# Kernel tuning notes

Measured on AMD Instinct MI355X. Metric: run time of the kernel, lower is better.

The kernel has to match this reference:

```python
import jax, jax.numpy as jnp
import numpy as np
import math

N_HEADS = 16
D_HEAD = 64
D_MODEL = 1024
ROPE_THETA = 10000.0


def setup_inputs() -> dict:
    key = jax.random.key(0)
    k1, k2, k3 = jax.random.split(key, 3)
    B, T = 2, 2048
    x = jax.random.normal(k1, (B, T, D_MODEL), dtype=jnp.float32)
    # torch Linear(in, out) weight has shape (out, in); store transposed (in, out)
    # so forward is x @ w. Scale like default init to keep activations sane.
    w_qkv = jax.random.normal(k2, (D_MODEL, 3 * D_MODEL), dtype=jnp.float32) / math.sqrt(D_MODEL)
    w_o = jax.random.normal(k3, (D_MODEL, D_MODEL), dtype=jnp.float32) / math.sqrt(D_MODEL)
    return {"x": x, "w_qkv": w_qkv, "w_o": w_o}


def _build_rope(T, dtype):
    inv_freq = 1.0 / (ROPE_THETA ** (jnp.arange(0, D_HEAD, 2, dtype=jnp.float32) / D_HEAD))
    t = jnp.arange(T, dtype=jnp.float32)
    freqs = jnp.outer(t, inv_freq)            # [T, D_HEAD/2]
    emb = jnp.concatenate([freqs, freqs], -1)  # [T, D_HEAD]
    return jnp.cos(emb).astype(dtype), jnp.sin(emb).astype(dtype)


def _apply_rope(x, cos, sin):
    # x: [B, T, H, D_HEAD]; cos/sin broadcast as [1, T, 1, D_HEAD]
    x1, x2 = jnp.split(x, 2, axis=-1)
    rotated = jnp.concatenate([-x2, x1], axis=-1)
    return x * cos + rotated * sin


def reference(x, w_qkv, w_o):
    B, T, D = x.shape
    qkv = (x @ w_qkv).reshape(B, T, 3, N_HEADS, D_HEAD)
    q, k, v = qkv[:, :, 0], qkv[:, :, 1], qkv[:, :, 2]  # [B, T, H, Dh]
    cos, sin = _build_rope(T, x.dtype)
    cos = cos[None, :, None, :]
    sin = sin[None, :, None, :]
    q = _apply_rope(q, cos, sin)
    k = _apply_rope(k, cos, sin)
    scale = 1.0 / math.sqrt(D_HEAD)
    # full [B, H, T, T] scores (faithful to the manual matmul-softmax-matmul)
    attn = jnp.einsum("bthd,bshd->bhts", q, k) * scale
    attn = jax.nn.softmax(attn, axis=-1)
    out = jnp.einsum("bhts,bshd->bthd", attn, v).reshape(B, T, D)
    return out @ w_o
```

## Files before the change

### kernel.cpp

```cpp
#include <hip/hip_runtime.h>
#include <cstdint>

typedef unsigned short ushort_t;
typedef __attribute__((ext_vector_type(8))) short v8s;
typedef __attribute__((ext_vector_type(4))) short v4s;
typedef __attribute__((ext_vector_type(2))) unsigned v2u;
typedef __attribute__((ext_vector_type(4))) float v4f;

#define MFMA(a, b, c) __builtin_amdgcn_mfma_f32_16x16x32_bf16(a, b, c, 0, 0, 0)
#define QSCALE 0.18033688011112042f

#define GLL(gp, lp) __builtin_amdgcn_global_load_lds(                        \
    (const __attribute__((address_space(1))) void*)(gp),                     \
    (__attribute__((address_space(3))) void*)(lp), 16, 0, 0)

__device__ __forceinline__ float bf2f(ushort_t u) {
    union { unsigned u; float f; } x; x.u = ((unsigned)u) << 16; return x.f;
}
__device__ __forceinline__ short f2bf(float f) {
    union { float f; unsigned u; } x; x.f = f;
    unsigned r = x.u + 0x7fffu + ((x.u >> 16) & 1u);
    return (short)(r >> 16);
}

__global__ __launch_bounds__(256) void prep(const void* __restrict__ xin,
                                            const void* __restrict__ w1,
                                            const void* __restrict__ w2,
                                            ushort_t* __restrict__ xb,
                                            ushort_t* __restrict__ out1,
                                            ushort_t* __restrict__ out2,
                                            int* __restrict__ flag,
                                            float* __restrict__ tab) {
    __shared__ ushort_t tile[64][65];
    __shared__ int cnt;
    int bid = blockIdx.x, tid = threadIdx.x;

    int isbf = 0;
    if (bid < 3072 || bid == 3328) {
        if (tid == 0) cnt = 0;
        __syncthreads();
        unsigned w = ((const unsigned*)xin)[tid];
        int e = (w >> 7) & 0xFF;
        int hit = ((e >= 96 && e <= 135) || (w & 0xFFFFu) == 0) ? 1 : 0;
        atomicAdd(&cnt, hit);
        __syncthreads();
        isbf = (cnt >= 160) ? 1 : 0;
        if (bid == 3328) {
            if (tid == 0) *flag = isbf;
            return;
        }
    }

    if (bid < 2048) {
        int i = bid * 256 + tid;
        if (isbf) {
            ((v8s*)xb)[i] = ((const v8s*)xin)[i];
        } else {
            const float* xf = (const float*)xin + (size_t)i * 8;
            v8s o;
            #pragma unroll
            for (int j = 0; j < 8; ++j) o[j] = f2bf(xf[j]);
            ((v8s*)xb)[i] = o;
        }
    } else if (bid < 3072) {
        int t = bid - 2048;
        int bxl = t & 63, by = (t >> 6) * 64;
        const void* in; ushort_t* out; int C, bx;
        if (bxl < 48) { in = w1; out = out1; C = 3072; bx = bxl * 64; }
        else          { in = w2; out = out2; C = 1024; bx = (bxl - 48) * 64; }
        const int R = 1024;
        int tx = tid & 63, ty = tid >> 6;
        for (int i = ty; i < 64; i += 4) {
            size_t idx = (size_t)(by + i) * C + bx + tx;
            tile[i][tx] = isbf ? ((const ushort_t*)in)[idx]
                               : (ushort_t)f2bf(((const float*)in)[idx]);
        }
        __syncthreads();
        for (int i = ty; i < 64; i += 4) out[(size_t)(bx + i) * R + by + tx] = tile[tx][i];
    } else {
        int idx = (bid - 3072) * 256 + tid;
        int t = idx >> 5, d = idx & 31;
        float inv_freq = __expf(-(float)d * 0.28782313662425575f);
        float ang = (float)t * inv_freq;
        float sn, cs;
        sincosf(ang, &sn, &cs);
        tab[t * 64 + d]      = bf2f((ushort_t)f2bf(cs));
        tab[t * 64 + 32 + d] = bf2f((ushort_t)f2bf(sn));
    }
}

template <int MODE, int BN>
__global__ __launch_bounds__(256) void gemm_bt(const ushort_t* __restrict__ A,
                                               const ushort_t* __restrict__ BT,
                                               void* __restrict__ C,
                                               const int* __restrict__ flagp,
                                               int M, int N, int K,
                                               ushort_t* __restrict__ Qp,
                                               ushort_t* __restrict__ Kp,
                                               ushort_t* __restrict__ Vp,
                                               const float* __restrict__ tab) {
    constexpr int NJ = BN / 32;
    __shared__ __align__(16) ushort_t As[2][128 * 32];
    __shared__ __align__(16) ushort_t Bs[2][BN * 32];
    int tid = threadIdx.x;
    int lane = tid & 63;
    int lr = lane & 15, lc = lane >> 4;
    int w = tid >> 6;
    int wr = (w >> 1) * 64, wc = (w & 1) * (BN / 2);

    int nx = gridDim.x;
    int orig = blockIdx.y * nx + blockIdx.x;
    int cpx = (nx * gridDim.y) >> 3;
    int swz = (orig & 7) * cpx + (orig >> 3);
    int m0 = (swz / nx) * 128, n0 = (swz % nx) * BN;

    int c0 = tid, c1 = tid + 256;
    int r0 = c0 >> 2, s0 = c0 & 3;
    int r1 = c1 >> 2, s1 = c1 & 3;

    const ushort_t* Ag0 = A + (size_t)(m0 + r0) * K + s0 * 8;
    const ushort_t* Ag1 = A + (size_t)(m0 + r1) * K + s1 * 8;
    const ushort_t* Bg0 = BT + (size_t)(n0 + r0) * K + s0 * 8;
    const ushort_t* Bg1 = BT + (size_t)(n0 + r1) * K + s1 * 8;
    const int aoff0 = w * 512;
    const int aoff1 = 2048 + w * 512;
    const int boff0 = w * 512;
    const int boff1 = 2048 + w * 512;

    v4f acc[4][NJ] = {};

    GLL(Ag0, &As[0][aoff0]);
    GLL(Ag1, &As[0][aoff1]);
    GLL(Bg0, &Bs[0][boff0]);
    if constexpr (BN == 128) GLL(Bg1, &Bs[0][boff1]);
    __syncthreads();

    int buf = 0;
    for (int kt = 0; kt < K; kt += 32) {
        if (kt + 32 < K) {
            int nb = buf ^ 1;
            GLL(Ag0 + kt + 32, &As[nb][aoff0]);
            GLL(Ag1 + kt + 32, &As[nb][aoff1]);
            GLL(Bg0 + kt + 32, &Bs[nb][boff0]);
            if constexpr (BN == 128) GLL(Bg1 + kt + 32, &Bs[nb][boff1]);
        }

        v8s af[4], bfr[NJ];
        #pragma unroll
        for (int i = 0; i < 4; ++i)
            af[i] = *(const v8s*)(&As[buf][0] + (wr + i * 16 + lr) * 32 + lc * 8);
        #pragma unroll
        for (int j = 0; j < NJ; ++j)
            bfr[j] = *(const v8s*)(&Bs[buf][0] + (wc + j * 16 + lr) * 32 + lc * 8);
        #pragma unroll
        for (int i = 0; i < 4; ++i)
            #pragma unroll
            for (int j = 0; j < NJ; ++j)
                acc[i][j] = MFMA(af[i], bfr[j], acc[i][j]);

        __syncthreads();
        buf ^= 1;
    }

    if (MODE == 1) {
        int store_f32 = (*flagp == 0);
        #pragma unroll
        for (int i = 0; i < 4; ++i)
            #pragma unroll
            for (int j = 0; j < NJ; ++j)
                #pragma unroll
                for (int r = 0; r < 4; ++r) {
                    int row = m0 + wr + i * 16 + lc * 4 + r;
                    int col = n0 + wc + j * 16 + lr;
                    if (store_f32)
                        ((float*)C)[(size_t)row * N + col] = acc[i][j][r];
                    else
                        ((ushort_t*)C)[(size_t)row * N + col] = (ushort_t)f2bf(acc[i][j][r]);
                }
    } else {
        int region = n0 >> 10;
        int h = ((n0 & 1023) + wc) >> 6;
        if (region < 2) {
            const float sc = (region == 0) ? QSCALE : 1.0f;
            ushort_t* dst = (region == 0) ? Qp : Kp;
            #pragma unroll
            for (int i = 0; i < 4; ++i)
                #pragma unroll
                for (int j = 0; j < 2; ++j) {
                    int d = j * 16 + lr;
                    #pragma unroll
                    for (int r = 0; r < 4; ++r) {
                        int tg = m0 + wr + i * 16 + lc * 4 + r;
                        int b = tg >> 11, tt = tg & 2047;
                        float cs = tab[tt * 64 + d], sn = tab[tt * 64 + 32 + d];
                        float x1 = acc[i][j][r], x2 = acc[i][(j + 2) % NJ][r];
                        size_t base = ((size_t)(b * 16 + h) * 2048 + tt) * 64 + d;
                        dst[base]      = (ushort_t)f2bf((x1 * cs - x2 * sn) * sc);
                        dst[base + 32] = (ushort_t)f2bf((x2 * cs + x1 * sn) * sc);
                    }
                }
        } else {
            #pragma unroll
            for (int i = 0; i < 4; ++i)
                #pragma unroll
                for (int j = 0; j < NJ; ++j) {
                    int d = j * 16 + lr;
                    int tg0 = m0 + wr + i * 16 + lc * 4;
                    int b = tg0 >> 11, tt = tg0 & 2047;
                    v4s pk;
                    #pragma unroll
                    for (int r = 0; r < 4; ++r) pk[r] = f2bf(acc[i][j][r]);
                    size_t base = (size_t)(b * 16 + h) * 131072 + (size_t)(tt >> 5) * 2048
                                + (size_t)d * 32 + (tt & 31);
                    *(v4s*)(Vp + base) = pk;
                }
        }
    }
}

__global__ __launch_bounds__(256) void attn(const ushort_t* __restrict__ Qr,
                                            const ushort_t* __restrict__ Kr,
                                            const ushort_t* __restrict__ Vt,
                                            ushort_t* __restrict__ AO) {
    __shared__ __align__(16) char lds[53248];
    int tid = threadIdx.x, lane = tid & 63, W = tid >> 6;
    int lr = lane & 15, lc = lane >> 4;
    int qsub = W & 1, sh = W >> 1;
    int L = blockIdx.x;
    int bh = (L & 7) * 4 + ((L >> 3) & 3);
    int qt = L >> 5;
    int q0 = qt * 128 + qsub * 64;
    int b = bh >> 4, h = bh & 15;
    const ushort_t* Qb = Qr + ((size_t)bh * 2048 + q0) * 64;
    const ushort_t* Kb = Kr + (size_t)bh * 131072 + (size_t)sh * 65536;
    const ushort_t* Vb = Vt + (size_t)bh * 131072 + (size_t)sh * 65536;
    ushort_t* Pw  = (ushort_t*)(lds + 32768 + W * 5120);
    ushort_t* KsG = (ushort_t*)(lds + sh * 16384);
    ushort_t* VsG = (ushort_t*)(lds + sh * 16384 + 8192);

    int gt = tid & 127;
    int c0 = gt, c1 = gt + 128;
    int kr0 = c0 >> 3, kc0 = c0 & 7, kr1 = c1 >> 3, kc1 = c1 & 7;
    const ushort_t* Kg0 = Kb + (size_t)kr0 * 64 + kc0 * 8;
    const ushort_t* Kg1 = Kb + (size_t)kr1 * 64 + kc1 * 8;
    int kl0 = kr0 * 64 + (kc0 ^ (kr0 & 7)) * 8;
    int kl1 = kr1 * 64 + (kc1 ^ (kr1 & 7)) * 8;
    const ushort_t* Vg0 = Vb + (size_t)c0 * 8;
    const ushort_t* Vg1 = Vb + (size_t)c1 * 8;
    int vl0 = c0 * 8, vl1 = c1 * 8;

    v8s qf[4][2];
    #pragma unroll
    for (int jq = 0; jq < 4; ++jq)
        #pragma unroll
        for (int kk = 0; kk < 2; ++kk)
            qf[jq][kk] = *(const v8s*)(Qb + (size_t)(jq * 16 + lr) * 64 + kk * 32 + lc * 8);

    v4f o[4][4] = {};
    float li[4] = {0.f, 0.f, 0.f, 0.f};

    v8s ka = *(const v8s*)(Kg0), kb2 = *(const v8s*)(Kg1);
    v8s va = *(const v8s*)(Vg0), vb2 = *(const v8s*)(Vg1);
    *(v8s*)(KsG + kl0) = ka;
    *(v8s*)(KsG + kl1) = kb2;
    *(v8s*)(VsG + vl0) = va;
    *(v8s*)(VsG + vl1) = vb2;
    ka  = *(const v8s*)(Kg0 + 2048);
    kb2 = *(const v8s*)(Kg1 + 2048);
    va  = *(const v8s*)(Vg0 + 2048);
    vb2 = *(const v8s*)(Vg1 + 2048);
    __syncthreads();

    #pragma unroll 1
    for (int t = 0; t < 32; ++t) {
        int p = t & 1;
        const ushort_t* Kl = KsG + p * 2048;
        const ushort_t* Vl = VsG + p * 2048;

        v8s kf[2][2], vf[4];
        #pragma unroll
        for (int hh = 0; hh < 2; ++hh)
            #pragma unroll
            for (int kk = 0; kk < 2; ++kk)
                kf[hh][kk] = *(const v8s*)(Kl + (hh * 16 + lr) * 64 + (((kk * 4 + lc) ^ (lr & 7)) * 8));
        #pragma unroll
        for (int i = 0; i < 4; ++i)
            vf[i] = *(const v8s*)(Vl + (i * 16 + lr) * 32 + lc * 8);

        v4f St[2][4] = {};
        __builtin_amdgcn_s_setprio(1);
        #pragma unroll
        for (int hh = 0; hh < 2; ++hh)
            #pragma unroll
            for (int jq = 0; jq < 4; ++jq) {
                St[hh][jq] = MFMA(kf[hh][0], qf[jq][0], St[hh][jq]);
                St[hh][jq] = MFMA(kf[hh][1], qf[jq][1], St[hh][jq]);
            }
        __builtin_amdgcn_s_setprio(0);

        if (t + 1 < 32) {
            ushort_t* Kn = KsG + (p ^ 1) * 2048;
            ushort_t* Vn = VsG + (p ^ 1) * 2048;
            *(v8s*)(Kn + kl0) = ka;
            *(v8s*)(Kn + kl1) = kb2;
            *(v8s*)(Vn + vl0) = va;
            *(v8s*)(Vn + vl1) = vb2;
        }
        if (t + 2 < 32) {
            ka  = *(const v8s*)(Kg0 + (size_t)(t + 2) * 2048);
            kb2 = *(const v8s*)(Kg1 + (size_t)(t + 2) * 2048);
            va  = *(const v8s*)(Vg0 + (size_t)(t + 2) * 2048);
            vb2 = *(const v8s*)(Vg1 + (size_t)(t + 2) * 2048);
        }

        #pragma unroll
        for (int jq = 0; jq < 4; ++jq)
            #pragma unroll
            for (int hh = 0; hh < 2; ++hh) {
                #pragma unroll
                for (int r = 0; r < 4; ++r) {
                    float ev = __builtin_amdgcn_exp2f(St[hh][jq][r]);
                    St[hh][jq][r] = ev;
                    li[jq] += ev;
                }
                unsigned d0 = __builtin_amdgcn_perm(__float_as_uint(St[hh][jq][1]),
                                                    __float_as_uint(St[hh][jq][0]), 0x07060302u);
                unsigned d1 = __builtin_amdgcn_perm(__float_as_uint(St[hh][jq][3]),
                                                    __float_as_uint(St[hh][jq][2]), 0x07060302u);
                v2u pk = {d0, d1};
                *(v2u*)(Pw + (jq * 16 + lr) * 40 + hh * 16 + lc * 4) = pk;
            }
        __builtin_amdgcn_s_waitcnt(0xc07f);
        __builtin_amdgcn_s_setprio(1);
        #pragma unroll
        for (int jq = 0; jq < 4; ++jq) {
            v8s pf = *(const v8s*)(Pw + (jq * 16 + lr) * 40 + lc * 8);
            #pragma unroll
            for (int i = 0; i < 4; ++i)
                o[i][jq] = MFMA(vf[i], pf, o[i][jq]);
        }
        __builtin_amdgcn_s_setprio(0);
        __syncthreads();
    }

    #pragma unroll
    for (int jq = 0; jq < 4; ++jq) {
        li[jq] += __shfl_xor(li[jq], 16);
        li[jq] += __shfl_xor(li[jq], 32);
    }
    float* MO = (float*)(lds + qsub * 17408);
    float* Ml = (float*)(lds + 34816 + qsub * 256);
    __syncthreads();
    if (sh == 1) {
        #pragma unroll
        for (int jq = 0; jq < 4; ++jq) {
            #pragma unroll
            for (int i = 0; i < 4; ++i)
                *(v4f*)(MO + (jq * 16 + lr) * 68 + i * 16 + lc * 4) = o[i][jq];
            if (lc == 0) Ml[jq * 16 + lr] = li[jq];
        }
    }
    __syncthreads();
    if (sh == 0) {
        #pragma unroll
        for (int jq = 0; jq < 4; ++jq) {
            float inv = 1.0f / (li[jq] + Ml[jq * 16 + lr]);
            int t = q0 + jq * 16 + lr;
            #pragma unroll
            for (int i = 0; i < 4; ++i) {
                v4f m = *(const v4f*)(MO + (jq * 16 + lr) * 68 + i * 16 + lc * 4);
                v4s pk;
                #pragma unroll
                for (int r = 0; r < 4; ++r) pk[r] = f2bf((o[i][jq][r] + m[r]) * inv);
                *(v4s*)(AO + (size_t)(b * 2048 + t) * 1024 + h * 64 + i * 16 + lc * 4) = pk;
            }
        }
    }
}

extern "C" void kernel_launch(void* const* d_in, const int* in_sizes, int n_in,
                              void* d_out, int out_size, void* d_ws, size_t ws_size,
                              hipStream_t stream) {
    char* ws = (char*)d_ws;
    int*      flag  = (int*)ws;
    ushort_t* wqkvT = (ushort_t*)(ws + 256);
    ushort_t* woT   = (ushort_t*)(ws + 6291712);
    ushort_t* xb    = (ushort_t*)(ws + 8388864);
    ushort_t* Qr    = (ushort_t*)(ws + 16777472);
    ushort_t* Kr    = (ushort_t*)(ws + 25166080);
    ushort_t* Vt    = (ushort_t*)(ws + 33554688);
    ushort_t* AO    = (ushort_t*)(ws + 41943296);
    float*    tab   = (float*)(ws + 50331904);

    prep<<<3329, 256, 0, stream>>>(d_in[0], d_in[1], d_in[2], xb, wqkvT, woT, flag, tab);
    gemm_bt<2, 128><<<dim3(24, 32), 256, 0, stream>>>(xb, wqkvT, nullptr, flag, 4096, 3072, 1024,
                                                      Qr, Kr, Vt, tab);
    attn<<<512, 256, 0, stream>>>(Qr, Kr, Vt, AO);
    gemm_bt<1, 64><<<dim3(16, 32), 256, 0, stream>>>(AO, woT, d_out, flag, 4096, 1024, 1024,
                                                     nullptr, nullptr, nullptr, nullptr);
}
```

Before: 192.9 us.

## Add dedicated 256x256-tile 8-wave QKV GEMM with staged LDS prefetch and XCD swizzle

Replaces the generic 128x128 QKV projection GEMM with a new 512-thread kernel using 256x256 output tiles, BK=64, swizzled LDS layout and interleaved global-to-LDS prefetch split across MFMA phases, plus a block-index remap so neighbouring tiles share cache. The RoPE/scale epilogue and V transpose are carried over. The attention loop's __syncthreads is replaced by an explicit LGKM wait plus raw barrier. The larger tile raises operand reuse but launches only 192 blocks on a 256-CU part and uses large LDS and register footprints.

```diff
diff --git a/kernel.cpp b/kernel.cpp
--- a/kernel.cpp
+++ b/kernel.cpp
@@ -13,6 +13,9 @@
 #define GLL(gp, lp) __builtin_amdgcn_global_load_lds(                        \
     (const __attribute__((address_space(1))) void*)(gp),                     \
     (__attribute__((address_space(3))) void*)(lp), 16, 0, 0)
+
+#define WAIT_LGKM0() __builtin_amdgcn_s_waitcnt(0xc07f)
+#define WAIT_VM0()   __builtin_amdgcn_s_waitcnt(0x3f70)
 
 __device__ __forceinline__ float bf2f(ushort_t u) {
     union { unsigned u; float f; } x; x.u = ((unsigned)u) << 16; return x.f;
@@ -86,6 +89,169 @@
         sincosf(ang, &sn, &cs);
         tab[t * 64 + d]      = bf2f((ushort_t)f2bf(cs));
         tab[t * 64 + 32 + d] = bf2f((ushort_t)f2bf(sn));
+    }
+}
+
+__global__ __launch_bounds__(512) void gemm_qkv(const ushort_t* __restrict__ A,
+                                                const ushort_t* __restrict__ BT,
+                                                ushort_t* __restrict__ Qp,
+                                                ushort_t* __restrict__ Kp,
+                                                ushort_t* __restrict__ Vp,
+                                                const float* __restrict__ tab) {
+    constexpr int K = 1024, NT = 16;
+    __shared__ __align__(16) ushort_t As[2][256 * 64];
+    __shared__ __align__(16) ushort_t Bs[2][256 * 64];
+    int tid = threadIdx.x, lane = tid & 63, w = tid >> 6;
+    int lr = lane & 15, lc = lane >> 4;
+    int lc_sw8 = (lc ^ ((lr & 4) >> 1)) * 8;
+    int wm = w >> 2, wn = w & 3;
+
+    int nx = gridDim.x;
+    int orig = blockIdx.y * nx + blockIdx.x;
+    int cpx = (nx * gridDim.y) >> 3;
+    int swz = (orig & 7) * cpx + (orig >> 3);
+    int m0 = (swz / nx) * 256, n0 = (swz % nx) * 256;
+
+    const ushort_t* ag[4]; const ushort_t* bg[4]; int lof[4];
+    #pragma unroll
+    for (int q = 0; q < 4; ++q) {
+        int ca = w * 64 + lane + q * 512;
+        int r = ca >> 3, s = (ca & 7) ^ ((r & 4) >> 1);
+        ag[q] = A  + (size_t)(m0 + r) * K + s * 8;
+        bg[q] = BT + (size_t)(n0 + r) * K + s * 8;
+        lof[q] = (w * 64 + q * 512) * 8;
+    }
+
+    v4f acc[8][4] = {};
+
+    #pragma unroll
+    for (int q = 0; q < 4; ++q) GLL(ag[q], &As[0][lof[q]]);
+    #pragma unroll
+    for (int q = 0; q < 4; ++q) GLL(bg[q], &Bs[0][lof[q]]);
+    WAIT_VM0();
+    __syncthreads();
+
+    #pragma unroll 1
+    for (int t = 0; t < NT; ++t) {
+        const ushort_t* Al = &As[t & 1][0];
+        const ushort_t* Bl = &Bs[t & 1][0];
+        ushort_t* An = &As[(t & 1) ^ 1][0];
+        ushort_t* Bn = &Bs[(t & 1) ^ 1][0];
+        int kg = (t + 1) * 64;
+
+        v8s a[4][2], b0[2][2], b1[2][2];
+        #pragma unroll
+        for (int i = 0; i < 4; ++i)
+            #pragma unroll
+            for (int kk = 0; kk < 2; ++kk)
+                a[i][kk] = *(const v8s*)(Al + (wm * 128 + i * 16 + lr) * 64 + kk * 32 + lc_sw8);
+        #pragma unroll
+        for (int j = 0; j < 2; ++j)
+            #pragma unroll
+            for (int kk = 0; kk < 2; ++kk)
+                b0[j][kk] = *(const v8s*)(Bl + (wn * 64 + j * 16 + lr) * 64 + kk * 32 + lc_sw8);
+        if (t + 1 < NT) {
+            #pragma unroll
+            for (int q = 0; q < 4; ++q) GLL(ag[q] + kg, An + lof[q]);
+        }
+        __builtin_amdgcn_s_setprio(1);
+        #pragma unroll
+        for (int i = 0; i < 4; ++i)
+            #pragma unroll
+            for (int j = 0; j < 2; ++j) {
+                acc[i][j] = MFMA(a[i][0], b0[j][0], acc[i][j]);
+                acc[i][j] = MFMA(a[i][1], b0[j][1], acc[i][j]);
+            }
+        __builtin_amdgcn_s_setprio(0);
+        __builtin_amdgcn_s_barrier();
+
+        #pragma unroll
+        for (int j = 0; j < 2; ++j)
+            #pragma unroll
+            for (int kk = 0; kk < 2; ++kk)
+                b1[j][kk] = *(const v8s*)(Bl + (wn * 64 + (j + 2) * 16 + lr) * 64 + kk * 32 + lc_sw8);
+        if (t + 1 < NT) {
+            #pragma unroll
+            for (int q = 0; q < 4; ++q) GLL(bg[q] + kg, Bn + lof[q]);
+        }
+        __builtin_amdgcn_s_setprio(1);
+        #pragma unroll
+        for (int i = 0; i < 4; ++i)
+            #pragma unroll
+            for (int j = 0; j < 2; ++j) {
+                acc[i][j + 2] = MFMA(a[i][0], b1[j][0], acc[i][j + 2]);
+                acc[i][j + 2] = MFMA(a[i][1], b1[j][1], acc[i][j + 2]);
+            }
+        __builtin_amdgcn_s_setprio(0);
+        __builtin_amdgcn_s_barrier();
+
+        #pragma unroll
+        for (int i = 0; i < 4; ++i)
+            #pragma unroll
+            for (int kk = 0; kk < 2; ++kk)
+                a[i][kk] = *(const v8s*)(Al + (wm * 128 + (i + 4) * 16 + lr) * 64 + kk * 32 + lc_sw8);
+        __builtin_amdgcn_s_setprio(1);
+        #pragma unroll
+        for (int i = 0; i < 4; ++i)
+            #pragma unroll
+            for (int j = 0; j < 2; ++j) {
+                acc[i + 4][j + 2] = MFMA(a[i][0], b1[j][0], acc[i + 4][j + 2]);
+                acc[i + 4][j + 2] = MFMA(a[i][1], b1[j][1], acc[i + 4][j + 2]);
+            }
+        __builtin_amdgcn_s_setprio(0);
+        __builtin_amdgcn_s_barrier();
+
+        __builtin_amdgcn_s_setprio(1);
+        #pragma unroll
+        for (int i = 0; i < 4; ++i)
+            #pragma unroll
+            for (int j = 0; j < 2; ++j) {
+                acc[i + 4][j] = MFMA(a[i][0], b0[j][0], acc[i + 4][j]);
+                acc[i + 4][j] = MFMA(a[i][1], b0[j][1], acc[i + 4][j]);
+            }
+        __builtin_amdgcn_s_setprio(0);
+        if (t + 1 < NT) {
+            WAIT_VM0();
+            __builtin_amdgcn_s_barrier();
+        }
+    }
+
+    int region = n0 >> 10;
+    int h = ((n0 & 1023) >> 6) + wn;
+    if (region < 2) {
+        const float sc = (region == 0) ? QSCALE : 1.0f;
+        ushort_t* dst = (region == 0) ? Qp : Kp;
+        #pragma unroll
+        for (int i = 0; i < 8; ++i)
+            #pragma unroll
+            for (int j = 0; j < 2; ++j) {
+                int d = j * 16 + lr;
+                #pragma unroll
+                for (int r = 0; r < 4; ++r) {
+                    int tg = m0 + wm * 128 + i * 16 + lc * 4 + r;
+                    int b = tg >> 11, tt = tg & 2047;
+                    float cs = tab[tt * 64 + d], sn = tab[tt * 64 + 32 + d];
+                    float x1 = acc[i][j][r], x2 = acc[i][j + 2][r];
+                    size_t base = ((size_t)(b * 16 + h) * 2048 + tt) * 64 + d;
+                    dst[base]      = (ushort_t)f2bf((x1 * cs - x2 * sn) * sc);
+                    dst[base + 32] = (ushort_t)f2bf((x2 * cs + x1 * sn) * sc);
+                }
+            }
+    } else {
+        #pragma unroll
+        for (int i = 0; i < 8; ++i)
+            #pragma unroll
+            for (int j = 0; j < 4; ++j) {
+                int d = j * 16 + lr;
+                int tg0 = m0 + wm * 128 + i * 16 + lc * 4;
+                int b = tg0 >> 11, tt = tg0 & 2047;
+                v4s pk;
+                #pragma unroll
+                for (int r = 0; r < 4; ++r) pk[r] = f2bf(acc[i][j][r]);
+                size_t base = (size_t)(b * 16 + h) * 131072 + (size_t)(tt >> 5) * 2048
+                            + (size_t)d * 32 + (tt & 31);
+                *(v4s*)(Vp + base) = pk;
+            }
     }
 }
 
@@ -177,44 +343,6 @@
                     else
                         ((ushort_t*)C)[(size_t)row * N + col] = (ushort_t)f2bf(acc[i][j][r]);
                 }
-    } else {
-        int region = n0 >> 10;
-        int h = ((n0 & 1023) + wc) >> 6;
-        if (region < 2) {
-            const float sc = (region == 0) ? QSCALE : 1.0f;
-            ushort_t* dst = (region == 0) ? Qp : Kp;
-            #pragma unroll
-            for (int i = 0; i < 4; ++i)
-                #pragma unroll
-                for (int j = 0; j < 2; ++j) {
-                    int d = j * 16 + lr;
-                    #pragma unroll
-                    for (int r = 0; r < 4; ++r) {
-                        int tg = m0 + wr + i * 16 + lc * 4 + r;
-                        int b = tg >> 11, tt = tg & 2047;
-                        float cs = tab[tt * 64 + d], sn = tab[tt * 64 + 32 + d];
-                        float x1 = acc[i][j][r], x2 = acc[i][(j + 2) % NJ][r];
-                        size_t base = ((size_t)(b * 16 + h) * 2048 + tt) * 64 + d;
-                        dst[base]      = (ushort_t)f2bf((x1 * cs - x2 * sn) * sc);
-                        dst[base + 32] = (ushort_t)f2bf((x2 * cs + x1 * sn) * sc);
-                    }
-                }
-        } else {
-            #pragma unroll
-            for (int i = 0; i < 4; ++i)
-                #pragma unroll
-                for (int j = 0; j < NJ; ++j) {
-                    int d = j * 16 + lr;
-                    int tg0 = m0 + wr + i * 16 + lc * 4;
-                    int b = tg0 >> 11, tt = tg0 & 2047;
-                    v4s pk;
-                    #pragma unroll
-                    for (int r = 0; r < 4; ++r) pk[r] = f2bf(acc[i][j][r]);
-                    size_t base = (size_t)(b * 16 + h) * 131072 + (size_t)(tt >> 5) * 2048
-                                + (size_t)d * 32 + (tt & 31);
-                    *(v4s*)(Vp + base) = pk;
-                }
-        }
     }
 }
 
@@ -330,7 +458,7 @@
                 v2u pk = {d0, d1};
                 *(v2u*)(Pw + (jq * 16 + lr) * 40 + hh * 16 + lc * 4) = pk;
             }
-        __builtin_amdgcn_s_waitcnt(0xc07f);
+        WAIT_LGKM0();
         __builtin_amdgcn_s_setprio(1);
         #pragma unroll
         for (int jq = 0; jq < 4; ++jq) {
@@ -340,7 +468,8 @@
                 o[i][jq] = MFMA(vf[i], pf, o[i][jq]);
         }
         __builtin_amdgcn_s_setprio(0);
-        __syncthreads();
+        WAIT_LGKM0();
+        __builtin_amdgcn_s_barrier();
     }
 
     #pragma unroll
@@ -393,8 +522,7 @@
     float*    tab   = (float*)(ws + 50331904);
 
     prep<<<3329, 256, 0, stream>>>(d_in[0], d_in[1], d_in[2], xb, wqkvT, woT, flag, tab);
-    gemm_bt<2, 128><<<dim3(24, 32), 256, 0, stream>>>(xb, wqkvT, nullptr, flag, 4096, 3072, 1024,
-                                                      Qr, Kr, Vt, tab);
+    gemm_qkv<<<dim3(12, 16), 512, 0, stream>>>(xb, wqkvT, Qr, Kr, Vt, tab);
     attn<<<512, 256, 0, stream>>>(Qr, Kr, Vt, AO);
     gemm_bt<1, 64><<<dim3(16, 32), 256, 0, stream>>>(AO, woT, d_out, flag, 4096, 1024, 1024,
                                                      nullptr, nullptr, nullptr, nullptr);
```

New measurement: 194.1 us. No clear change (+0.6%).
